# Kernel tuning notes

Measured on AMD Instinct MI355X. Metric: run time of the kernel, lower is better.

The kernel has to match this reference:

```python
import jax, jax.numpy as jnp
import numpy as np

BETA = 0.95
THR = 1.0
NUM_STEPS = 100
ALPHA = 2.0  # snntorch atan surrogate default

@jax.custom_vjp
def atan_spike(x):
    return (x > 0).astype(x.dtype)

def _as_fwd(x):
    return (x > 0).astype(x.dtype), x

def _as_bwd(x, g):
    return (g * (ALPHA / 2) / (1 + (jnp.pi / 2 * ALPHA * x) ** 2),)

atan_spike.defvjp(_as_fwd, _as_bwd)


def setup_inputs() -> dict:
    key = jax.random.key(0)
    ks = jax.random.split(key, 9)
    B = 16384
    SH, NH, CO, OUT = 1024, 1024, 256, 64
    s = 0.05
    return {
        "x": jax.random.normal(ks[0], (B, 105), jnp.float32),
        "snn_w1": jax.random.normal(ks[1], (SH, 5), jnp.float32) * s,
        "snn_b1": jnp.zeros((SH,), jnp.float32),
        "snn_w2": jax.random.normal(ks[2], (OUT, SH), jnp.float32) * s,
        "snn_b2": jnp.zeros((OUT,), jnp.float32),
        "nn_w1": jax.random.normal(ks[3], (NH, 5), jnp.float32) * s,
        "nn_b1": jnp.zeros((NH,), jnp.float32),
        "nn_w2": jax.random.normal(ks[4], (OUT, NH), jnp.float32) * s,
        "nn_b2": jnp.zeros((OUT,), jnp.float32),
        "conv_w": jax.random.normal(ks[5], (32, 1, 3), jnp.float32) * s,
        "conv_b": jnp.zeros((32,), jnp.float32),
        "cnn_fc_w": jax.random.normal(ks[6], (CO, 32 * 50), jnp.float32) * s,
        "cnn_fc_b": jnp.zeros((CO,), jnp.float32),
        "comb_w": jax.random.normal(ks[7], (OUT, 2 * OUT + CO), jnp.float32) * s,
        "comb_b": jnp.zeros((OUT,), jnp.float32),
    }


def _forward(x, snn_w1, snn_b1, snn_w2, snn_b2, nn_w1, nn_b1, nn_w2, nn_b2,
             conv_w, conv_b, cnn_fc_w, cnn_fc_b, comb_w, comb_b):
    feats = x[:, :5]                 # [B,5]
    wave = x[:, 5:][:, None, :]      # [B,1,100]
    B = x.shape[0]

    # ---- SNN branch (LIF, beta leak, subtract reset, threshold 1.0) ----
    cur1 = feats @ snn_w1.T + snn_b1  # input current is constant across steps

    def step(carry, _):
        mem1, spk1, mem2, spk2 = carry
        # reset term uses detached spike (snntorch mem_reset detaches)
        mem1 = BETA * mem1 + cur1 - jax.lax.stop_gradient(spk1) * THR
        spk1 = atan_spike(mem1 - THR)
        cur2 = spk1 @ snn_w2.T + snn_b2
        mem2 = BETA * mem2 + cur2 - jax.lax.stop_gradient(spk2) * THR
        spk2 = atan_spike(mem2 - THR)
        return (mem1, spk1, mem2, spk2), spk2

    z1 = jnp.zeros_like(cur1)
    z2 = jnp.zeros((B, snn_w2.shape[0]), cur1.dtype)
    _, spk_rec = jax.lax.scan(step, (z1, z1, z2, z2), None, length=NUM_STEPS)
    snn_out = spk_rec.mean(axis=0)   # [B,OUT]

    # ---- MLP branch ----
    nn_out = jax.nn.relu(feats @ nn_w1.T + nn_b1) @ nn_w2.T + nn_b2

    # ---- CNN branch ----
    c = jax.lax.conv_general_dilated(wave, conv_w, (1,), [(1, 1)],
                                     dimension_numbers=("NCW", "OIW", "NCW"))
    c = jax.nn.relu(c + conv_b[None, :, None])   # [B,32,100]
    c = c.reshape(B, 32, 50, 2).max(axis=-1)      # MaxPool1d(k=2,s=2)
    cnn_out = c.reshape(B, -1) @ cnn_fc_w.T + cnn_fc_b

    combined = jnp.concatenate([snn_out, nn_out, cnn_out], axis=1)
    return combined @ comb_w.T + comb_b


def reference(x, snn_w1, snn_b1, snn_w2, snn_b2, nn_w1, nn_b1, nn_w2, nn_b2,
              conv_w, conv_b, cnn_fc_w, cnn_fc_b, comb_w, comb_b):
    return _forward(x, snn_w1, snn_b1, snn_w2, snn_b2, nn_w1, nn_b1, nn_w2,
                    nn_b2, conv_w, conv_b, cnn_fc_w, cnn_fc_b, comb_w, comb_b)
```

## Files before the change

### kernel.cpp

```cpp
#include <hip/hip_runtime.h>

typedef __bf16 bf16x8_t __attribute__((ext_vector_type(8)));
typedef float f32x4_t __attribute__((ext_vector_type(4)));
typedef float f32x2_t __attribute__((ext_vector_type(2)));

#define NSTEPS 100
#define PB0 0u
#define PB1 32768u
#define COMBF 51200u

static __device__ __forceinline__ unsigned short f2bfu(float v) {
  union { __bf16 h; unsigned short u; } c; c.h = (__bf16)v; return c.u;
}
static __device__ __forceinline__ unsigned int pack2bf(float a, float b) {
  return (unsigned)f2bfu(a) | ((unsigned)f2bfu(b) << 16);
}
union BF8U { unsigned int u[4]; bf16x8_t v; };

static __device__ __forceinline__ f32x2_t pk_mul(f32x2_t a, f32x2_t b) {
  f32x2_t d; asm("v_pk_mul_f32 %0, %1, %2" : "=v"(d) : "v"(a), "v"(b)); return d;
}
static __device__ __forceinline__ f32x2_t pk_add(f32x2_t a, f32x2_t b) {
  f32x2_t d; asm("v_pk_add_f32 %0, %1, %2" : "=v"(d) : "v"(a), "v"(b)); return d;
}

static __device__ __forceinline__ bf16x8_t bfrag_f32(const float* __restrict__ p, float s) {
  BF8U r;
#pragma unroll
  for (int i = 0; i < 4; ++i) r.u[i] = pack2bf(p[2*i]*s, p[2*i+1]*s);
  return r.v;
}

static __device__ __forceinline__ void comb_store(unsigned char* ldsp, int k, int row, float v) {
  *(unsigned short*)(ldsp + COMBF +
      (unsigned)((k >> 5)*1024 + (((k >> 3) & 3)*16 + row)*16 + (k & 7)*2)) = f2bfu(v);
}

__global__ __launch_bounds__(512, 2)
void hybrid_v5(const float* __restrict__ x,
               const float* __restrict__ snn_w1, const float* __restrict__ snn_b1,
               const float* __restrict__ snn_w2, const float* __restrict__ snn_b2,
               const float* __restrict__ nn_w1,  const float* __restrict__ nn_b1,
               const float* __restrict__ nn_w2,  const float* __restrict__ nn_b2,
               const float* __restrict__ conv_w, const float* __restrict__ conv_b,
               const float* __restrict__ fc_w,   const float* __restrict__ fc_b,
               const float* __restrict__ comb_w, const float* __restrict__ comb_b,
               const unsigned short* __restrict__ fcwb, int use_bf,
               float* __restrict__ out)
{
  __shared__ __align__(16) unsigned char lds[65536];
  const int tid  = threadIdx.x;
  const int w    = tid >> 6;
  const int l    = tid & 63;
  const int q    = l >> 4;
  const int m    = l & 15;
  const int row0 = blockIdx.x * 16;

  const int hi  = w >> 2;
  const int ntr = w & 3;
  const int rn  = ntr*16 + m;
  const int rA  = hi*4 + q;

  const float* xr = x + (row0 + m)*105;
  const float f0 = xr[0], f1 = xr[1], f2 = xr[2], f3 = xr[3], f4 = xr[4];
  const float b2l = snn_b2[rn];

  bf16x8_t bfr[4][4];
#pragma unroll
  for (int ci = 0; ci < 4; ++ci)
#pragma unroll
    for (int nt = 0; nt < 4; ++nt)
      bfr[ci][nt] = bfrag_f32(snn_w2 + (nt*16 + m)*1024 + (w*4 + ci)*32 + q*8, 1.f);

  f32x2_t c2[16], mem2[16], spneg2[16];
  f32x2_t beta2; beta2.x = 0.95f; beta2.y = 0.95f;
  {
    const int kb = w*128 + q*8;
#pragma unroll
    for (int ci = 0; ci < 4; ++ci) {
      const float* wp = snn_w1 + (kb + ci*32)*5;
      float wa[40];
#pragma unroll
      for (int u2 = 0; u2 < 10; ++u2) {
        const float4 t4 = *(const float4*)(wp + u2*4);
        wa[u2*4+0] = t4.x; wa[u2*4+1] = t4.y; wa[u2*4+2] = t4.z; wa[u2*4+3] = t4.w;
      }
      float cc[8];
#pragma unroll
      for (int j = 0; j < 8; ++j)
        cc[j] = f0*wa[j*5] + f1*wa[j*5+1] + f2*wa[j*5+2] + f3*wa[j*5+3] + f4*wa[j*5+4]
              + snn_b1[kb + ci*32 + j];
#pragma unroll
      for (int jj = 0; jj < 4; ++jj) {
        f32x2_t t; t.x = cc[2*jj]; t.y = cc[2*jj+1];
        c2[ci*4+jj] = t;
        f32x2_t z; z.x = 0.f; z.y = 0.f;
        mem2[ci*4+jj] = z;
        f32x2_t nz; nz.x = -0.0f; nz.y = -0.0f;
        spneg2[ci*4+jj] = nz;
      }
    }
  }

  BF8U afr[4];
  auto lif_update_pack = [&]() {
#pragma unroll
    for (int i = 0; i < 16; ++i) {
      const f32x2_t mk = pk_add(pk_add(pk_mul(mem2[i], beta2), c2[i]), spneg2[i]);
      mem2[i] = mk;
      f32x2_t sn;
      sn.x = mk.x > 1.f ? -1.0f : -0.0f;
      sn.y = mk.y > 1.f ? -1.0f : -0.0f;
      spneg2[i] = sn;
      afr[i>>2].u[i&3] =
          __builtin_amdgcn_perm(__float_as_uint(sn.y), __float_as_uint(sn.x), 0x07060302u)
          & 0x3F803F80u;
    }
  };
  lif_update_pack();

  f32x2_t m2;     m2.x = 0.f;     m2.y = 0.f;
  f32x2_t s2neg;  s2neg.x = -0.0f; s2neg.y = -0.0f;
  f32x2_t cntneg; cntneg.x = 0.f; cntneg.y = 0.f;
  f32x2_t sbias2; sbias2.x = b2l; sbias2.y = b2l;

  const unsigned wbase = (unsigned)(w*4096 + (q&1)*2048 + (q>>1)*4 + m*8);
  const unsigned rbase = (unsigned)(rA*512 + rn*8);
  const f32x4_t z4 = {0.f, 0.f, 0.f, 0.f};

  auto lif2 = [&](f32x2_t cur2) {
    m2 = pk_add(pk_add(pk_mul(m2, beta2), cur2), s2neg);
    f32x2_t sn;
    sn.x = m2.x > 1.f ? -1.0f : -0.0f;
    sn.y = m2.y > 1.f ? -1.0f : -0.0f;
    s2neg = sn;
    cntneg = pk_add(cntneg, sn);
  };

  auto phase = [&](unsigned cur, unsigned prv, bool doRead, bool doLif) {
    f32x2_t v2[8];
    if (doRead)
#pragma unroll
      for (int s = 0; s < 8; ++s)
        v2[s] = *(const f32x2_t*)(lds + prv + rbase + (unsigned)(s*4096));
    f32x4_t acc[4] = {z4, z4, z4, z4};
#pragma unroll
    for (int ci = 0; ci < 4; ++ci)
#pragma unroll
      for (int nt = 0; nt < 4; ++nt)
        acc[nt] = __builtin_amdgcn_mfma_f32_16x16x32_bf16(afr[ci].v, bfr[ci][nt], acc[nt], 0,0,0);
#pragma unroll
    for (int nt = 0; nt < 4; ++nt)
#pragma unroll
      for (int r = 0; r < 4; ++r)
        *(float*)(lds + cur + wbase + (unsigned)(r*512 + nt*128)) = acc[nt][r];
    if (doLif) lif_update_pack();
    if (doRead) {
      const f32x2_t t = pk_add(pk_add(pk_add(v2[0],v2[1]), pk_add(v2[2],v2[3])),
                               pk_add(pk_add(v2[4],v2[5]), pk_add(v2[6],v2[7])));
      lif2(pk_add(t, sbias2));
    }
    __syncthreads();
  };

#pragma unroll 1
  for (int tt = 0; tt < NSTEPS; tt += 2) {
    phase(PB0, PB1, tt > 0, true);
    phase(PB1, PB0, true,  tt + 1 < NSTEPS - 1);
  }

#pragma unroll
  for (int ci = 0; ci < 4; ++ci)
#pragma unroll
    for (int nt = 0; nt < 4; ++nt)
      bfr[ci][nt] = bfrag_f32(nn_w2 + (nt*16 + m)*1024 + (w*4 + ci)*32 + q*8, 1.f);
  {
    f32x2_t v2[8];
#pragma unroll
    for (int s = 0; s < 8; ++s)
      v2[s] = *(const f32x2_t*)(lds + PB1 + rbase + (unsigned)(s*4096));
    const f32x2_t t = pk_add(pk_add(pk_add(v2[0],v2[1]), pk_add(v2[2],v2[3])),
                             pk_add(pk_add(v2[4],v2[5]), pk_add(v2[6],v2[7])));
    lif2(pk_add(t, sbias2));

    BF8U hfr[4];
    const int kb = w*128 + q*8;
#pragma unroll
    for (int ci = 0; ci < 4; ++ci) {
      const float* wp = nn_w1 + (kb + ci*32)*5;
      float wa[40];
#pragma unroll
      for (int u2 = 0; u2 < 10; ++u2) {
        const float4 t4 = *(const float4*)(wp + u2*4);
        wa[u2*4+0] = t4.x; wa[u2*4+1] = t4.y; wa[u2*4+2] = t4.z; wa[u2*4+3] = t4.w;
      }
      float hv[8];
#pragma unroll
      for (int j = 0; j < 8; ++j) {
        const float h = f0*wa[j*5] + f1*wa[j*5+1] + f2*wa[j*5+2] + f3*wa[j*5+3] + f4*wa[j*5+4]
                      + nn_b1[kb + ci*32 + j];
        hv[j] = fmaxf(h, 0.f);
      }
#pragma unroll
      for (int jj = 0; jj < 4; ++jj) hfr[ci].u[jj] = pack2bf(hv[2*jj], hv[2*jj+1]);
    }
    f32x4_t acc[4] = {z4, z4, z4, z4};
#pragma unroll
    for (int ci = 0; ci < 4; ++ci)
#pragma unroll
      for (int nt = 0; nt < 4; ++nt)
        acc[nt] = __builtin_amdgcn_mfma_f32_16x16x32_bf16(hfr[ci].v, bfr[ci][nt], acc[nt], 0,0,0);
#pragma unroll
    for (int nt = 0; nt < 4; ++nt)
#pragma unroll
      for (int r = 0; r < 4; ++r)
        *(float*)(lds + PB0 + wbase + (unsigned)(r*512 + nt*128)) = acc[nt][r];
  }
  __syncthreads();
  {
    f32x2_t v2[8];
#pragma unroll
    for (int s = 0; s < 8; ++s)
      v2[s] = *(const f32x2_t*)(lds + PB0 + rbase + (unsigned)(s*4096));
    const f32x2_t t = pk_add(pk_add(pk_add(v2[0],v2[1]), pk_add(v2[2],v2[3])),
                             pk_add(pk_add(v2[4],v2[5]), pk_add(v2[6],v2[7])));
    const float nb = nn_b2[rn];
    f32x2_t nb2; nb2.x = nb; nb2.y = nb;
    const f32x2_t n2 = pk_add(t, nb2);
    comb_store(lds, rn,      rA,     cntneg.x * -0.0078125f);
    comb_store(lds, rn,      rA + 8, cntneg.y * -0.0078125f);
    comb_store(lds, 64 + rn, rA,     n2.x);
    comb_store(lds, 64 + rn, rA + 8, n2.y);
  }
  __syncthreads();

  {
    const int ch = tid >> 4;
    const float cw0 = conv_w[ch*3+0], cw1 = conv_w[ch*3+1], cw2 = conv_w[ch*3+2];
    const float cbb = conv_b[ch];
    const float* xw = xr + 5;
    float xm1 = 0.f, x0v = xw[0];
#pragma unroll 1
    for (int p = 0; p < 50; ++p) {
      const float xp1 = xw[2*p + 1];
      const float xp2 = (p < 49) ? xw[2*p + 2] : 0.f;
      const float av = cw0*xm1 + cw1*x0v + cw2*xp1 + cbb;
      const float bv = cw0*x0v + cw1*xp1 + cw2*xp2 + cbb;
      const float pv = fmaxf(fmaxf(av, 0.f), fmaxf(bv, 0.f));
      const int k = ch*50 + p;
      *(unsigned short*)(lds + (unsigned)((k>>5)*1024 + (((k>>3)&3)*16 + m)*16 + (k&7)*2)) = f2bfu(pv);
      xm1 = xp1; x0v = xp2;
    }
  }
  __syncthreads();

  {
    const int c0 = (w*2 + 0)*16 + m;
    const int c1 = (w*2 + 1)*16 + m;
    f32x4_t e0 = z4, o0 = z4, e1 = z4, o1 = z4;
    if (use_bf) {
#pragma unroll 2
      for (int kc = 0; kc < 50; kc += 2) {
        const bf16x8_t a0 = *(const bf16x8_t*)(lds + (unsigned)((kc*64 + l)*16));
        const bf16x8_t a1 = *(const bf16x8_t*)(lds + (unsigned)(((kc+1)*64 + l)*16));
        e0 = __builtin_amdgcn_mfma_f32_16x16x32_bf16(a0, *(const bf16x8_t*)(fcwb + c0*1600 + kc*32 + q*8), e0, 0,0,0);
        o0 = __builtin_amdgcn_mfma_f32_16x16x32_bf16(a1, *(const bf16x8_t*)(fcwb + c0*1600 + (kc+1)*32 + q*8), o0, 0,0,0);
        e1 = __builtin_amdgcn_mfma_f32_16x16x32_bf16(a0, *(const bf16x8_t*)(fcwb + c1*1600 + kc*32 + q*8), e1, 0,0,0);
        o1 = __builtin_amdgcn_mfma_f32_16x16x32_bf16(a1, *(const bf16x8_t*)(fcwb + c1*1600 + (kc+1)*32 + q*8), o1, 0,0,0);
      }
    } else {
#pragma unroll 2
      for (int kc = 0; kc < 50; kc += 2) {
        const bf16x8_t a0 = *(const bf16x8_t*)(lds + (unsigned)((kc*64 + l)*16));
        const bf16x8_t a1 = *(const bf16x8_t*)(lds + (unsigned)(((kc+1)*64 + l)*16));
        e0 = __builtin_amdgcn_mfma_f32_16x16x32_bf16(a0, bfrag_f32(fc_w + c0*1600 + kc*32 + q*8, 1.f), e0, 0,0,0);
        o0 = __builtin_amdgcn_mfma_f32_16x16x32_bf16(a1, bfrag_f32(fc_w + c0*1600 + (kc+1)*32 + q*8, 1.f), o0, 0,0,0);
        e1 = __builtin_amdgcn_mfma_f32_16x16x32_bf16(a0, bfrag_f32(fc_w + c1*1600 + kc*32 + q*8, 1.f), e1, 0,0,0);
        o1 = __builtin_amdgcn_mfma_f32_16x16x32_bf16(a1, bfrag_f32(fc_w + c1*1600 + (kc+1)*32 + q*8, 1.f), o1, 0,0,0);
      }
    }
    const float fb0 = fc_b[c0], fb1 = fc_b[c1];
#pragma unroll
    for (int r = 0; r < 4; ++r) {
      comb_store(lds, 128 + c0, q*4 + r, (e0[r] + o0[r]) + fb0);
      comb_store(lds, 128 + c1, q*4 + r, (e1[r] + o1[r]) + fb1);
    }
  }
  __syncthreads();

  if (w < 4) {
    const int cn = w*16 + m;
    f32x4_t oe = z4, oo = z4;
#pragma unroll
    for (int kc = 0; kc < 12; kc += 2) {
      const bf16x8_t a0 = *(const bf16x8_t*)(lds + COMBF + (unsigned)((kc*64 + l)*16));
      const bf16x8_t a1 = *(const bf16x8_t*)(lds + COMBF + (unsigned)(((kc+1)*64 + l)*16));
      const float s0 = (kc    < 2) ? 1.28f : 1.f;
      const float s1 = (kc+1 < 2) ? 1.28f : 1.f;
      oe = __builtin_amdgcn_mfma_f32_16x16x32_bf16(a0, bfrag_f32(comb_w + cn*384 + kc*32 + q*8, s0), oe, 0,0,0);
      oo = __builtin_amdgcn_mfma_f32_16x16x32_bf16(a1, bfrag_f32(comb_w + cn*384 + (kc+1)*32 + q*8, s1), oo, 0,0,0);
    }
    const float cb2 = comb_b[cn];
#pragma unroll
    for (int r = 0; r < 4; ++r)
      out[(row0 + q*4 + r)*64 + cn] = (oe[r] + oo[r]) + cb2;
  }
}

__global__ __launch_bounds__(256)
void fcw_to_bf16(const float* __restrict__ src, unsigned short* __restrict__ dst) {
  const int i = (blockIdx.x * 256 + threadIdx.x) * 4;
  const float4 v = *(const float4*)(src + i);
  ushort4 o;
  o.x = f2bfu(v.x); o.y = f2bfu(v.y); o.z = f2bfu(v.z); o.w = f2bfu(v.w);
  *(ushort4*)(dst + i) = o;
}

extern "C" void kernel_launch(void* const* d_in, const int* in_sizes, int n_in,
                              void* d_out, int out_size, void* d_ws, size_t ws_size,
                              hipStream_t stream) {
  const float* x       = (const float*)d_in[0];
  const float* snn_w1  = (const float*)d_in[1];
  const float* snn_b1  = (const float*)d_in[2];
  const float* snn_w2  = (const float*)d_in[3];
  const float* snn_b2  = (const float*)d_in[4];
  const float* nn_w1   = (const float*)d_in[5];
  const float* nn_b1   = (const float*)d_in[6];
  const float* nn_w2   = (const float*)d_in[7];
  const float* nn_b2   = (const float*)d_in[8];
  const float* conv_w  = (const float*)d_in[9];
  const float* conv_b  = (const float*)d_in[10];
  const float* fc_w    = (const float*)d_in[11];
  const float* fc_b    = (const float*)d_in[12];
  const float* comb_w  = (const float*)d_in[13];
  const float* comb_b  = (const float*)d_in[14];
  float* outp = (float*)d_out;

  const int rows = in_sizes[0] / 105;
  const int grid = rows / 16;

  const size_t fcw_elems = (size_t)in_sizes[11];
  const int use_bf = (ws_size >= fcw_elems * 2) ? 1 : 0;
  unsigned short* fcwb = (unsigned short*)d_ws;
  if (use_bf) {
    fcw_to_bf16<<<dim3((unsigned)(fcw_elems / 1024)), dim3(256), 0, stream>>>(fc_w, fcwb);
  }

  hybrid_v5<<<dim3(grid), dim3(512), 0, stream>>>(
      x, snn_w1, snn_b1, snn_w2, snn_b2,
      nn_w1, nn_b1, nn_w2, nn_b2,
      conv_w, conv_b, fc_w, fc_b, comb_w, comb_b,
      fcwb, use_bf, outp);
}
```

Baseline: 684.7 us.

## Batch four LIF timesteps per barrier using quadruple-buffered LDS partials

Computes layer-1 spikes for four timesteps ahead, storing packed spike fragments in a 4-deep register array. It then issues four MFMA groups into four LDS slices before a single barrier and reduces all four layer-2 updates afterwards. This removes most of the per-step __syncthreads overhead in the 100-step scan. LDS doubles to 128KB, which likely limits residency to one block per CU, and register usage grows. Packed-math helpers are also rewritten as in-place asm.

```diff
diff --git a/kernel.cpp b/kernel.cpp
--- a/kernel.cpp
+++ b/kernel.cpp
@@ -5,8 +5,6 @@
 typedef float f32x2_t __attribute__((ext_vector_type(2)));
 
 #define NSTEPS 100
-#define PB0 0u
-#define PB1 32768u
 #define COMBF 51200u
 
 static __device__ __forceinline__ unsigned short f2bfu(float v) {
@@ -17,11 +15,11 @@
 }
 union BF8U { unsigned int u[4]; bf16x8_t v; };
 
-static __device__ __forceinline__ f32x2_t pk_mul(f32x2_t a, f32x2_t b) {
-  f32x2_t d; asm("v_pk_mul_f32 %0, %1, %2" : "=v"(d) : "v"(a), "v"(b)); return d;
-}
-static __device__ __forceinline__ f32x2_t pk_add(f32x2_t a, f32x2_t b) {
-  f32x2_t d; asm("v_pk_add_f32 %0, %1, %2" : "=v"(d) : "v"(a), "v"(b)); return d;
+static __device__ __forceinline__ void pk_mul_ip(f32x2_t &a, f32x2_t b) {
+  asm("v_pk_mul_f32 %0, %0, %1" : "+v"(a) : "v"(b));
+}
+static __device__ __forceinline__ void pk_add_ip(f32x2_t &a, f32x2_t b) {
+  asm("v_pk_add_f32 %0, %0, %1" : "+v"(a) : "v"(b));
 }
 
 static __device__ __forceinline__ bf16x8_t bfrag_f32(const float* __restrict__ p, float s) {
@@ -37,7 +35,7 @@
 }
 
 __global__ __launch_bounds__(512, 2)
-void hybrid_v5(const float* __restrict__ x,
+void hybrid_v6(const float* __restrict__ x,
                const float* __restrict__ snn_w1, const float* __restrict__ snn_b1,
                const float* __restrict__ snn_w2, const float* __restrict__ snn_b2,
                const float* __restrict__ nn_w1,  const float* __restrict__ nn_b1,
@@ -48,7 +46,7 @@
                const unsigned short* __restrict__ fcwb, int use_bf,
                float* __restrict__ out)
 {
-  __shared__ __align__(16) unsigned char lds[65536];
+  __shared__ __align__(16) unsigned char lds[131072];
   const int tid  = threadIdx.x;
   const int w    = tid >> 6;
   const int l    = tid & 63;
@@ -72,7 +70,7 @@
     for (int nt = 0; nt < 4; ++nt)
       bfr[ci][nt] = bfrag_f32(snn_w2 + (nt*16 + m)*1024 + (w*4 + ci)*32 + q*8, 1.f);
 
-  f32x2_t c2[16], mem2[16], spneg2[16];
+  f32x2_t c2[16], mem2[16];
   f32x2_t beta2; beta2.x = 0.95f; beta2.y = 0.95f;
   {
     const int kb = w*128 + q*8;
@@ -96,77 +94,93 @@
         c2[ci*4+jj] = t;
         f32x2_t z; z.x = 0.f; z.y = 0.f;
         mem2[ci*4+jj] = z;
-        f32x2_t nz; nz.x = -0.0f; nz.y = -0.0f;
-        spneg2[ci*4+jj] = nz;
-      }
-    }
-  }
-
-  BF8U afr[4];
-  auto lif_update_pack = [&]() {
+      }
+    }
+  }
+
+  BF8U afr[4][4];
+#pragma unroll
+  for (int ci = 0; ci < 4; ++ci)
+#pragma unroll
+    for (int j = 0; j < 4; ++j) afr[3][ci].u[j] = 0u;
+
+  auto lif_step = [&](int pi, int po) {
 #pragma unroll
     for (int i = 0; i < 16; ++i) {
-      const f32x2_t mk = pk_add(pk_add(pk_mul(mem2[i], beta2), c2[i]), spneg2[i]);
-      mem2[i] = mk;
+      const unsigned pw = afr[pi][i>>2].u[i&3];
       f32x2_t sn;
-      sn.x = mk.x > 1.f ? -1.0f : -0.0f;
-      sn.y = mk.y > 1.f ? -1.0f : -0.0f;
-      spneg2[i] = sn;
-      afr[i>>2].u[i&3] =
-          __builtin_amdgcn_perm(__float_as_uint(sn.y), __float_as_uint(sn.x), 0x07060302u)
-          & 0x3F803F80u;
+      sn.x = __uint_as_float((pw << 16) | 0x80000000u);
+      sn.y = __uint_as_float((pw & 0x3F800000u) | 0x80000000u);
+      pk_mul_ip(mem2[i], beta2);
+      pk_add_ip(mem2[i], c2[i]);
+      pk_add_ip(mem2[i], sn);
+      const unsigned lo  = mem2[i].x > 1.f ? 0x3F80u     : 0u;
+      const unsigned hi2 = mem2[i].y > 1.f ? 0x3F800000u : 0u;
+      afr[po][i>>2].u[i&3] = lo | hi2;
     }
   };
-  lif_update_pack();
-
-  f32x2_t m2;     m2.x = 0.f;     m2.y = 0.f;
+  lif_step(3,0); lif_step(0,1); lif_step(1,2); lif_step(2,3);
+
+  f32x2_t m2;     m2.x = 0.f;      m2.y = 0.f;
   f32x2_t s2neg;  s2neg.x = -0.0f; s2neg.y = -0.0f;
-  f32x2_t cntneg; cntneg.x = 0.f; cntneg.y = 0.f;
-  f32x2_t sbias2; sbias2.x = b2l; sbias2.y = b2l;
+  f32x2_t cntneg; cntneg.x = 0.f;  cntneg.y = 0.f;
+  f32x2_t sbias2; sbias2.x = b2l;  sbias2.y = b2l;
 
   const unsigned wbase = (unsigned)(w*4096 + (q&1)*2048 + (q>>1)*4 + m*8);
   const unsigned rbase = (unsigned)(rA*512 + rn*8);
   const f32x4_t z4 = {0.f, 0.f, 0.f, 0.f};
 
-  auto lif2 = [&](f32x2_t cur2) {
-    m2 = pk_add(pk_add(pk_mul(m2, beta2), cur2), s2neg);
-    f32x2_t sn;
-    sn.x = m2.x > 1.f ? -1.0f : -0.0f;
-    sn.y = m2.y > 1.f ? -1.0f : -0.0f;
-    s2neg = sn;
-    cntneg = pk_add(cntneg, sn);
+  auto reduce_lif2 = [&](f32x2_t v[8]) {
+    pk_add_ip(v[0], v[1]); pk_add_ip(v[2], v[3]);
+    pk_add_ip(v[4], v[5]); pk_add_ip(v[6], v[7]);
+    pk_add_ip(v[0], v[2]); pk_add_ip(v[4], v[6]);
+    pk_add_ip(v[0], v[4]);
+    pk_add_ip(v[0], sbias2);
+    pk_mul_ip(m2, beta2);
+    pk_add_ip(m2, v[0]);
+    pk_add_ip(m2, s2neg);
+    s2neg.x = m2.x > 1.f ? -1.0f : -0.0f;
+    s2neg.y = m2.y > 1.f ? -1.0f : -0.0f;
+    pk_add_ip(cntneg, s2neg);
   };
 
-  auto phase = [&](unsigned cur, unsigned prv, bool doRead, bool doLif) {
-    f32x2_t v2[8];
-    if (doRead)
-#pragma unroll
-      for (int s = 0; s < 8; ++s)
-        v2[s] = *(const f32x2_t*)(lds + prv + rbase + (unsigned)(s*4096));
-    f32x4_t acc[4] = {z4, z4, z4, z4};
-#pragma unroll
-    for (int ci = 0; ci < 4; ++ci)
+#pragma unroll 1
+  for (int ss = 0; ss < 25; ++ss) {
+#pragma unroll
+    for (int k = 0; k < 4; ++k) {
+      f32x4_t acc[4] = {z4, z4, z4, z4};
+#pragma unroll
+      for (int ci = 0; ci < 4; ++ci)
+#pragma unroll
+        for (int nt = 0; nt < 4; ++nt)
+          acc[nt] = __builtin_amdgcn_mfma_f32_16x16x32_bf16(afr[k][ci].v, bfr[ci][nt], acc[nt], 0,0,0);
+      unsigned char* wp = lds + (unsigned)(k*32768) + wbase;
 #pragma unroll
       for (int nt = 0; nt < 4; ++nt)
-        acc[nt] = __builtin_amdgcn_mfma_f32_16x16x32_bf16(afr[ci].v, bfr[ci][nt], acc[nt], 0,0,0);
-#pragma unroll
-    for (int nt = 0; nt < 4; ++nt)
-#pragma unroll
-      for (int r = 0; r < 4; ++r)
-        *(float*)(lds + cur + wbase + (unsigned)(r*512 + nt*128)) = acc[nt][r];
-    if (doLif) lif_update_pack();
-    if (doRead) {
-      const f32x2_t t = pk_add(pk_add(pk_add(v2[0],v2[1]), pk_add(v2[2],v2[3])),
-                               pk_add(pk_add(v2[4],v2[5]), pk_add(v2[6],v2[7])));
-      lif2(pk_add(t, sbias2));
+#pragma unroll
+        for (int r = 0; r < 4; ++r)
+          *(float*)(wp + (unsigned)(r*512 + nt*128)) = acc[nt][r];
     }
     __syncthreads();
-  };
-
-#pragma unroll 1
-  for (int tt = 0; tt < NSTEPS; tt += 2) {
-    phase(PB0, PB1, tt > 0, true);
-    phase(PB1, PB0, true,  tt + 1 < NSTEPS - 1);
+
+    {
+      const unsigned char* rp = lds + rbase;
+      f32x2_t va[8], vb[8];
+#pragma unroll
+      for (int s = 0; s < 8; ++s) va[s] = *(const f32x2_t*)(rp + (unsigned)(s*4096));
+#pragma unroll
+      for (int s = 0; s < 8; ++s) vb[s] = *(const f32x2_t*)(rp + 32768u + (unsigned)(s*4096));
+      if (ss < 24) { lif_step(3,0); lif_step(0,1); lif_step(1,2); lif_step(2,3); }
+      reduce_lif2(va);
+      reduce_lif2(vb);
+#pragma unroll
+      for (int s = 0; s < 8; ++s) va[s] = *(const f32x2_t*)(rp + 65536u + (unsigned)(s*4096));
+#pragma unroll
+      for (int s = 0; s < 8; ++s) vb[s] = *(const f32x2_t*)(rp + 98304u + (unsigned)(s*4096));
+      reduce_lif2(va);
+      reduce_lif2(vb);
+    }
+    __syncthreads();
   }
 
 #pragma unroll
@@ -175,14 +189,6 @@
     for (int nt = 0; nt < 4; ++nt)
       bfr[ci][nt] = bfrag_f32(nn_w2 + (nt*16 + m)*1024 + (w*4 + ci)*32 + q*8, 1.f);
   {
-    f32x2_t v2[8];
-#pragma unroll
-    for (int s = 0; s < 8; ++s)
-      v2[s] = *(const f32x2_t*)(lds + PB1 + rbase + (unsigned)(s*4096));
-    const f32x2_t t = pk_add(pk_add(pk_add(v2[0],v2[1]), pk_add(v2[2],v2[3])),
-                             pk_add(pk_add(v2[4],v2[5]), pk_add(v2[6],v2[7])));
-    lif2(pk_add(t, sbias2));
-
     BF8U hfr[4];
     const int kb = w*128 + q*8;
 #pragma unroll
@@ -214,23 +220,25 @@
     for (int nt = 0; nt < 4; ++nt)
 #pragma unroll
       for (int r = 0; r < 4; ++r)
-        *(float*)(lds + PB0 + wbase + (unsigned)(r*512 + nt*128)) = acc[nt][r];
+        *(float*)(lds + wbase + (unsigned)(r*512 + nt*128)) = acc[nt][r];
   }
   __syncthreads();
   {
-    f32x2_t v2[8];
-#pragma unroll
-    for (int s = 0; s < 8; ++s)
-      v2[s] = *(const f32x2_t*)(lds + PB0 + rbase + (unsigned)(s*4096));
-    const f32x2_t t = pk_add(pk_add(pk_add(v2[0],v2[1]), pk_add(v2[2],v2[3])),
-                             pk_add(pk_add(v2[4],v2[5]), pk_add(v2[6],v2[7])));
+    f32x2_t va[8];
+    const unsigned char* rp = lds + rbase;
+#pragma unroll
+    for (int s = 0; s < 8; ++s) va[s] = *(const f32x2_t*)(rp + (unsigned)(s*4096));
+    pk_add_ip(va[0], va[1]); pk_add_ip(va[2], va[3]);
+    pk_add_ip(va[4], va[5]); pk_add_ip(va[6], va[7]);
+    pk_add_ip(va[0], va[2]); pk_add_ip(va[4], va[6]);
+    pk_add_ip(va[0], va[4]);
     const float nb = nn_b2[rn];
     f32x2_t nb2; nb2.x = nb; nb2.y = nb;
-    const f32x2_t n2 = pk_add(t, nb2);
+    pk_add_ip(va[0], nb2);
     comb_store(lds, rn,      rA,     cntneg.x * -0.0078125f);
     comb_store(lds, rn,      rA + 8, cntneg.y * -0.0078125f);
-    comb_store(lds, 64 + rn, rA,     n2.x);
-    comb_store(lds, 64 + rn, rA + 8, n2.y);
+    comb_store(lds, 64 + rn, rA,     va[0].x);
+    comb_store(lds, 64 + rn, rA + 8, va[0].y);
   }
   __syncthreads();
 
@@ -346,7 +354,7 @@
     fcw_to_bf16<<<dim3((unsigned)(fcw_elems / 1024)), dim3(256), 0, stream>>>(fc_w, fcwb);
   }
 
-  hybrid_v5<<<dim3(grid), dim3(512), 0, stream>>>(
+  hybrid_v6<<<dim3(grid), dim3(512), 0, stream>>>(
       x, snn_w1, snn_b1, snn_w2, snn_b2,
       nn_w1, nn_b1, nn_w2, nn_b2,
       conv_w, conv_b, fc_w, fc_b, comb_w, comb_b,
```

Result: slower. 762.9 us (+11.4%).

## Split SNN hidden dimension across 16 waves with 1024-thread blocks

Applied to the files above, without the earlier changes.

Doubles the block size to 1024 threads so each wave owns 64 of the 1024 hidden neurons instead of 128, halving per-wave MFMA and LIF work per timestep. The reduction buffers grow to 64 KB each (128 KB total LDS), and the layer-2 LIF now reduces 16 partial sums per output lane in scalar form. Spike state is kept only in the packed bf16 A-fragments, which removes the separate negative-spike arrays and uses in-place packed ops. The CNN conv and FC stages are re-split over the extra waves. The larger LDS footprint and 1024-thread blocks may limit residency per CU, and the launch_bounds of (1024,4) is probably unachievable.

```diff
diff --git a/kernel.cpp b/kernel.cpp
--- a/kernel.cpp
+++ b/kernel.cpp
@@ -6,8 +6,8 @@
 
 #define NSTEPS 100
 #define PB0 0u
-#define PB1 32768u
-#define COMBF 51200u
+#define PB1 65536u
+#define COMBF 98304u
 
 static __device__ __forceinline__ unsigned short f2bfu(float v) {
   union { __bf16 h; unsigned short u; } c; c.h = (__bf16)v; return c.u;
@@ -17,11 +17,11 @@
 }
 union BF8U { unsigned int u[4]; bf16x8_t v; };
 
-static __device__ __forceinline__ f32x2_t pk_mul(f32x2_t a, f32x2_t b) {
-  f32x2_t d; asm("v_pk_mul_f32 %0, %1, %2" : "=v"(d) : "v"(a), "v"(b)); return d;
-}
-static __device__ __forceinline__ f32x2_t pk_add(f32x2_t a, f32x2_t b) {
-  f32x2_t d; asm("v_pk_add_f32 %0, %1, %2" : "=v"(d) : "v"(a), "v"(b)); return d;
+static __device__ __forceinline__ void pk_mul_ip(f32x2_t &a, f32x2_t b) {
+  asm("v_pk_mul_f32 %0, %0, %1" : "+v"(a) : "v"(b));
+}
+static __device__ __forceinline__ void pk_add_ip(f32x2_t &a, f32x2_t b) {
+  asm("v_pk_add_f32 %0, %0, %1" : "+v"(a) : "v"(b));
 }
 
 static __device__ __forceinline__ bf16x8_t bfrag_f32(const float* __restrict__ p, float s) {
@@ -36,8 +36,8 @@
       (unsigned)((k >> 5)*1024 + (((k >> 3) & 3)*16 + row)*16 + (k & 7)*2)) = f2bfu(v);
 }
 
-__global__ __launch_bounds__(512, 2)
-void hybrid_v5(const float* __restrict__ x,
+__global__ __launch_bounds__(1024, 4)
+void hybrid_v8(const float* __restrict__ x,
                const float* __restrict__ snn_w1, const float* __restrict__ snn_b1,
                const float* __restrict__ snn_w2, const float* __restrict__ snn_b2,
                const float* __restrict__ nn_w1,  const float* __restrict__ nn_b1,
@@ -48,7 +48,7 @@
                const unsigned short* __restrict__ fcwb, int use_bf,
                float* __restrict__ out)
 {
-  __shared__ __align__(16) unsigned char lds[65536];
+  __shared__ __align__(16) unsigned char lds[131072];
   const int tid  = threadIdx.x;
   const int w    = tid >> 6;
   const int l    = tid & 63;
@@ -56,28 +56,24 @@
   const int m    = l & 15;
   const int row0 = blockIdx.x * 16;
 
-  const int hi  = w >> 2;
-  const int ntr = w & 3;
-  const int rn  = ntr*16 + m;
-  const int rA  = hi*4 + q;
-
   const float* xr = x + (row0 + m)*105;
   const float f0 = xr[0], f1 = xr[1], f2 = xr[2], f3 = xr[3], f4 = xr[4];
-  const float b2l = snn_b2[rn];
-
-  bf16x8_t bfr[4][4];
-#pragma unroll
-  for (int ci = 0; ci < 4; ++ci)
+
+  const float b2l = snn_b2[l];
+
+  bf16x8_t bfr[2][4];
+#pragma unroll
+  for (int ci = 0; ci < 2; ++ci)
 #pragma unroll
     for (int nt = 0; nt < 4; ++nt)
-      bfr[ci][nt] = bfrag_f32(snn_w2 + (nt*16 + m)*1024 + (w*4 + ci)*32 + q*8, 1.f);
-
-  f32x2_t c2[16], mem2[16], spneg2[16];
+      bfr[ci][nt] = bfrag_f32(snn_w2 + (nt*16 + m)*1024 + (w*64 + ci*32) + q*8, 1.f);
+
+  f32x2_t c2[8], mem2[8];
   f32x2_t beta2; beta2.x = 0.95f; beta2.y = 0.95f;
   {
-    const int kb = w*128 + q*8;
-#pragma unroll
-    for (int ci = 0; ci < 4; ++ci) {
+    const int kb = w*64 + q*8;
+#pragma unroll 1
+    for (int ci = 0; ci < 2; ++ci) {
       const float* wp = snn_w1 + (kb + ci*32)*5;
       float wa[40];
 #pragma unroll
@@ -96,70 +92,70 @@
         c2[ci*4+jj] = t;
         f32x2_t z; z.x = 0.f; z.y = 0.f;
         mem2[ci*4+jj] = z;
-        f32x2_t nz; nz.x = -0.0f; nz.y = -0.0f;
-        spneg2[ci*4+jj] = nz;
-      }
-    }
-  }
-
-  BF8U afr[4];
-  auto lif_update_pack = [&]() {
-#pragma unroll
-    for (int i = 0; i < 16; ++i) {
-      const f32x2_t mk = pk_add(pk_add(pk_mul(mem2[i], beta2), c2[i]), spneg2[i]);
-      mem2[i] = mk;
+      }
+    }
+  }
+
+  BF8U afr[2];
+#pragma unroll
+  for (int ci = 0; ci < 2; ++ci)
+#pragma unroll
+    for (int j = 0; j < 4; ++j) afr[ci].u[j] = 0u;
+
+  auto lif_step = [&]() {
+#pragma unroll
+    for (int i = 0; i < 8; ++i) {
+      const unsigned pw = afr[i>>2].u[i&3];
       f32x2_t sn;
-      sn.x = mk.x > 1.f ? -1.0f : -0.0f;
-      sn.y = mk.y > 1.f ? -1.0f : -0.0f;
-      spneg2[i] = sn;
-      afr[i>>2].u[i&3] =
-          __builtin_amdgcn_perm(__float_as_uint(sn.y), __float_as_uint(sn.x), 0x07060302u)
-          & 0x3F803F80u;
+      sn.x = __uint_as_float((pw << 16) | 0x80000000u);
+      sn.y = __uint_as_float((pw & 0x3F800000u) | 0x80000000u);
+      pk_mul_ip(mem2[i], beta2);
+      pk_add_ip(mem2[i], c2[i]);
+      pk_add_ip(mem2[i], sn);
+      const unsigned lo  = mem2[i].x > 1.f ? 0x3F80u     : 0u;
+      const unsigned hi2 = mem2[i].y > 1.f ? 0x3F800000u : 0u;
+      afr[i>>2].u[i&3] = lo | hi2;
     }
   };
-  lif_update_pack();
-
-  f32x2_t m2;     m2.x = 0.f;     m2.y = 0.f;
-  f32x2_t s2neg;  s2neg.x = -0.0f; s2neg.y = -0.0f;
-  f32x2_t cntneg; cntneg.x = 0.f; cntneg.y = 0.f;
-  f32x2_t sbias2; sbias2.x = b2l; sbias2.y = b2l;
+  lif_step();
+
+  float m2 = 0.f, s2 = 0.f, cnt = 0.f;
 
   const unsigned wbase = (unsigned)(w*4096 + (q&1)*2048 + (q>>1)*4 + m*8);
-  const unsigned rbase = (unsigned)(rA*512 + rn*8);
+  const unsigned rbase = (unsigned)((w&7)*512 + (w>>3)*4 + l*8);
   const f32x4_t z4 = {0.f, 0.f, 0.f, 0.f};
 
-  auto lif2 = [&](f32x2_t cur2) {
-    m2 = pk_add(pk_add(pk_mul(m2, beta2), cur2), s2neg);
-    f32x2_t sn;
-    sn.x = m2.x > 1.f ? -1.0f : -0.0f;
-    sn.y = m2.y > 1.f ? -1.0f : -0.0f;
-    s2neg = sn;
-    cntneg = pk_add(cntneg, sn);
+  auto l2_update = [&](float cur) {
+    m2 = __fsub_rn(__fadd_rn(__fmul_rn(0.95f, m2), cur), s2);
+    s2 = m2 > 1.f ? 1.f : 0.f;  cnt += s2;
   };
+  auto tree16 = [&](const float* t) -> float {
+    const float a = (t[0]+t[1]) + (t[2]+t[3]);
+    const float b = (t[4]+t[5]) + (t[6]+t[7]);
+    const float c = (t[8]+t[9]) + (t[10]+t[11]);
+    const float d = (t[12]+t[13]) + (t[14]+t[15]);
+    return (a+b) + (c+d);
+  };
 
   auto phase = [&](unsigned cur, unsigned prv, bool doRead, bool doLif) {
-    f32x2_t v2[8];
+    float t[16];
     if (doRead)
 #pragma unroll
-      for (int s = 0; s < 8; ++s)
-        v2[s] = *(const f32x2_t*)(lds + prv + rbase + (unsigned)(s*4096));
+      for (int s = 0; s < 16; ++s)
+        t[s] = *(const float*)(lds + prv + rbase + (unsigned)(s*4096));
     f32x4_t acc[4] = {z4, z4, z4, z4};
 #pragma unroll
-    for (int ci = 0; ci < 4; ++ci)
+    for (int ci = 0; ci < 2; ++ci)
 #pragma unroll
       for (int nt = 0; nt < 4; ++nt)
         acc[nt] = __builtin_amdgcn_mfma_f32_16x16x32_bf16(afr[ci].v, bfr[ci][nt], acc[nt], 0,0,0);
+    if (doLif) lif_step();
 #pragma unroll
     for (int nt = 0; nt < 4; ++nt)
 #pragma unroll
       for (int r = 0; r < 4; ++r)
         *(float*)(lds + cur + wbase + (unsigned)(r*512 + nt*128)) = acc[nt][r];
-    if (doLif) lif_update_pack();
-    if (doRead) {
-      const f32x2_t t = pk_add(pk_add(pk_add(v2[0],v2[1]), pk_add(v2[2],v2[3])),
-                               pk_add(pk_add(v2[4],v2[5]), pk_add(v2[6],v2[7])));
-      lif2(pk_add(t, sbias2));
-    }
+    if (doRead) l2_update(tree16(t) + b2l);
     __syncthreads();
   };
 
@@ -170,23 +166,21 @@
   }
 
 #pragma unroll
-  for (int ci = 0; ci < 4; ++ci)
+  for (int ci = 0; ci < 2; ++ci)
 #pragma unroll
     for (int nt = 0; nt < 4; ++nt)
-      bfr[ci][nt] = bfrag_f32(nn_w2 + (nt*16 + m)*1024 + (w*4 + ci)*32 + q*8, 1.f);
-  {
-    f32x2_t v2[8];
-#pragma unroll
-    for (int s = 0; s < 8; ++s)
-      v2[s] = *(const f32x2_t*)(lds + PB1 + rbase + (unsigned)(s*4096));
-    const f32x2_t t = pk_add(pk_add(pk_add(v2[0],v2[1]), pk_add(v2[2],v2[3])),
-                             pk_add(pk_add(v2[4],v2[5]), pk_add(v2[6],v2[7])));
-    lif2(pk_add(t, sbias2));
-
-    BF8U hfr[4];
-    const int kb = w*128 + q*8;
-#pragma unroll
-    for (int ci = 0; ci < 4; ++ci) {
+      bfr[ci][nt] = bfrag_f32(nn_w2 + (nt*16 + m)*1024 + (w*64 + ci*32) + q*8, 1.f);
+  {
+    float t[16];
+#pragma unroll
+    for (int s = 0; s < 16; ++s)
+      t[s] = *(const float*)(lds + PB1 + rbase + (unsigned)(s*4096));
+    l2_update(tree16(t) + b2l);
+
+    BF8U hfr[2];
+    const int kb = w*64 + q*8;
+#pragma unroll 1
+    for (int ci = 0; ci < 2; ++ci) {
       const float* wp = nn_w1 + (kb + ci*32)*5;
       float wa[40];
 #pragma unroll
@@ -206,7 +200,7 @@
     }
     f32x4_t acc[4] = {z4, z4, z4, z4};
 #pragma unroll
-    for (int ci = 0; ci < 4; ++ci)
+    for (int ci = 0; ci < 2; ++ci)
 #pragma unroll
       for (int nt = 0; nt < 4; ++nt)
         acc[nt] = __builtin_amdgcn_mfma_f32_16x16x32_bf16(hfr[ci].v, bfr[ci][nt], acc[nt], 0,0,0);
@@ -218,30 +212,27 @@
   }
   __syncthreads();
   {
-    f32x2_t v2[8];
-#pragma unroll
-    for (int s = 0; s < 8; ++s)
-      v2[s] = *(const f32x2_t*)(lds + PB0 + rbase + (unsigned)(s*4096));
-    const f32x2_t t = pk_add(pk_add(pk_add(v2[0],v2[1]), pk_add(v2[2],v2[3])),
-                             pk_add(pk_add(v2[4],v2[5]), pk_add(v2[6],v2[7])));
-    const float nb = nn_b2[rn];
-    f32x2_t nb2; nb2.x = nb; nb2.y = nb;
-    const f32x2_t n2 = pk_add(t, nb2);
-    comb_store(lds, rn,      rA,     cntneg.x * -0.0078125f);
-    comb_store(lds, rn,      rA + 8, cntneg.y * -0.0078125f);
-    comb_store(lds, 64 + rn, rA,     n2.x);
-    comb_store(lds, 64 + rn, rA + 8, n2.y);
+    float t[16];
+#pragma unroll
+    for (int s = 0; s < 16; ++s)
+      t[s] = *(const float*)(lds + PB0 + rbase + (unsigned)(s*4096));
+    const float nnv = tree16(t) + nn_b2[l];
+    comb_store(lds, l,      w, cnt * 0.0078125f);
+    comb_store(lds, 64 + l, w, nnv);
   }
   __syncthreads();
 
   {
-    const int ch = tid >> 4;
+    const int g  = tid >> 9;
+    const int ch = (tid >> 4) & 31;
     const float cw0 = conv_w[ch*3+0], cw1 = conv_w[ch*3+1], cw2 = conv_w[ch*3+2];
     const float cbb = conv_b[ch];
     const float* xw = xr + 5;
-    float xm1 = 0.f, x0v = xw[0];
+    const int p0 = g*25;
+    float xm1 = (p0 == 0) ? 0.f : xw[2*p0 - 1];
+    float x0v = xw[2*p0];
 #pragma unroll 1
-    for (int p = 0; p < 50; ++p) {
+    for (int p = p0; p < p0 + 25; ++p) {
       const float xp1 = xw[2*p + 1];
       const float xp2 = (p < 49) ? xw[2*p + 2] : 0.f;
       const float av = cw0*xm1 + cw1*x0v + cw2*xp1 + cbb;
@@ -255,9 +246,8 @@
   __syncthreads();
 
   {
-    const int c0 = (w*2 + 0)*16 + m;
-    const int c1 = (w*2 + 1)*16 + m;
-    f32x4_t e0 = z4, o0 = z4, e1 = z4, o1 = z4;
+    const int c0 = w*16 + m;
+    f32x4_t e0 = z4, o0 = z4;
     if (use_bf) {
 #pragma unroll 2
       for (int kc = 0; kc < 50; kc += 2) {
@@ -265,8 +255,6 @@
         const bf16x8_t a1 = *(const bf16x8_t*)(lds + (unsigned)(((kc+1)*64 + l)*16));
         e0 = __builtin_amdgcn_mfma_f32_16x16x32_bf16(a0, *(const bf16x8_t*)(fcwb + c0*1600 + kc*32 + q*8), e0, 0,0,0);
         o0 = __builtin_amdgcn_mfma_f32_16x16x32_bf16(a1, *(const bf16x8_t*)(fcwb + c0*1600 + (kc+1)*32 + q*8), o0, 0,0,0);
-        e1 = __builtin_amdgcn_mfma_f32_16x16x32_bf16(a0, *(const bf16x8_t*)(fcwb + c1*1600 + kc*32 + q*8), e1, 0,0,0);
-        o1 = __builtin_amdgcn_mfma_f32_16x16x32_bf16(a1, *(const bf16x8_t*)(fcwb + c1*1600 + (kc+1)*32 + q*8), o1, 0,0,0);
       }
     } else {
 #pragma unroll 2
@@ -275,16 +263,12 @@
         const bf16x8_t a1 = *(const bf16x8_t*)(lds + (unsigned)(((kc+1)*64 + l)*16));
         e0 = __builtin_amdgcn_mfma_f32_16x16x32_bf16(a0, bfrag_f32(fc_w + c0*1600 + kc*32 + q*8, 1.f), e0, 0,0,0);
         o0 = __builtin_amdgcn_mfma_f32_16x16x32_bf16(a1, bfrag_f32(fc_w + c0*1600 + (kc+1)*32 + q*8, 1.f), o0, 0,0,0);
-        e1 = __builtin_amdgcn_mfma_f32_16x16x32_bf16(a0, bfrag_f32(fc_w + c1*1600 + kc*32 + q*8, 1.f), e1, 0,0,0);
-        o1 = __builtin_amdgcn_mfma_f32_16x16x32_bf16(a1, bfrag_f32(fc_w + c1*1600 + (kc+1)*32 + q*8, 1.f), o1, 0,0,0);
-      }
-    }
-    const float fb0 = fc_b[c0], fb1 = fc_b[c1];
-#pragma unroll
-    for (int r = 0; r < 4; ++r) {
+      }
+    }
+    const float fb0 = fc_b[c0];
+#pragma unroll
+    for (int r = 0; r < 4; ++r)
       comb_store(lds, 128 + c0, q*4 + r, (e0[r] + o0[r]) + fb0);
-      comb_store(lds, 128 + c1, q*4 + r, (e1[r] + o1[r]) + fb1);
-    }
   }
   __syncthreads();
 
@@ -346,7 +330,7 @@
     fcw_to_bf16<<<dim3((unsigned)(fcw_elems / 1024)), dim3(256), 0, stream>>>(fc_w, fcwb);
   }
 
-  hybrid_v5<<<dim3(grid), dim3(512), 0, stream>>>(
+  hybrid_v8<<<dim3(grid), dim3(1024), 0, stream>>>(
       x, snn_w1, snn_b1, snn_w2, snn_b2,
       nn_w1, nn_b1, nn_w2, nn_b2,
       conv_w, conv_b, fc_w, fc_b, comb_w, comb_b,
```

Measured after the change: 1.188 ms. 1.74x slower.
